# Kernel optimization log

Hardware: AMD Instinct MI355X
Metric: run time of the kernel (lower is better)

The kernel has to match this reference:

```python
import jax, jax.numpy as jnp
import numpy as np


def gcn_conv(x, W, b, src, dst, num_nodes):
    # PyG GCNConv: h = D^{-1/2} (A + I) D^{-1/2} (x W) + b
    h = x @ W  # [N, H]
    ones = jnp.ones(src.shape[0], dtype=h.dtype)
    deg = jax.ops.segment_sum(ones, dst, num_segments=num_nodes) + 1.0  # +1 for self-loop
    d_inv_sqrt = jax.lax.rsqrt(deg)
    norm = d_inv_sqrt[src] * d_inv_sqrt[dst]  # [E]
    msg = h[src] * norm[:, None]  # [E, H] gather
    agg = jax.ops.segment_sum(msg, dst, num_segments=num_nodes)  # scatter-add
    agg = agg + h * (1.0 / deg)[:, None]  # self-loop term: deg_i^{-1/2} * deg_i^{-1/2}
    return agg + b


def setup_inputs() -> dict:
    key = jax.random.key(0)
    ks = jax.random.split(key, 10)
    N, E, F, H, C, G = 100000, 1000000, 64, 128, 2, 512
    x = jax.random.normal(ks[0], (N, F), dtype=jnp.float32)
    edge_index = jax.random.randint(ks[1], (2, E), 0, N, dtype=jnp.int64)
    batch = jnp.sort(jax.random.randint(ks[2], (N,), 0, G, dtype=jnp.int64))
    s1 = 1.0 / np.sqrt(F)
    s2 = 1.0 / np.sqrt(H)
    W1 = jax.random.normal(ks[3], (F, H), dtype=jnp.float32) * s1
    b1 = jnp.zeros((H,), dtype=jnp.float32)
    W2 = jax.random.normal(ks[4], (H, H), dtype=jnp.float32) * s2
    b2 = jnp.zeros((H,), dtype=jnp.float32)
    Wfc = jax.random.normal(ks[5], (H, C), dtype=jnp.float32) * s2
    bfc = jnp.zeros((C,), dtype=jnp.float32)
    return {"x": x, "edge_index": edge_index, "batch": batch, "num_graphs": G,
            "W1": W1, "b1": b1, "W2": W2, "b2": b2, "Wfc": Wfc, "bfc": bfc}


def reference(x, edge_index, batch, num_graphs, W1, b1, W2, b2, Wfc, bfc):
    # Dropout is inference-mode (identity), matching model.eval().
    N = x.shape[0]
    src, dst = edge_index[0], edge_index[1]
    h = gcn_conv(x, W1, b1, src, dst, N)
    h = jax.nn.relu(h)
    h = gcn_conv(h, W2, b2, src, dst, N)
    h = jax.nn.relu(h)
    # global mean pool over graphs
    summed = jax.ops.segment_sum(h, batch, num_segments=num_graphs)  # [G, H]
    counts = jax.ops.segment_sum(jnp.ones((N,), h.dtype), batch, num_segments=num_graphs)
    pooled = summed / jnp.maximum(counts, 1.0)[:, None]
    logits = pooled @ Wfc + bfc  # [G, C]
    return jax.nn.softmax(logits, axis=1)
```

## Files before the change

### kernel.cpp

```cpp
#include <hip/hip_runtime.h>
#include <hip/hip_bf16.h>

typedef __hip_bfloat16 bf16;
typedef __attribute__((ext_vector_type(8))) short short8;
typedef __attribute__((ext_vector_type(4))) float f32x4;
typedef __attribute__((ext_vector_type(2))) float f32x2;

#define FDIM 64
#define HDIM 128
#define PROWS 256

#define ESTRIDE 4096
#define EC 8192
#define ECPT (EC / 256)

__device__ __forceinline__ float b2f(bf16 v) { return __bfloat162float(v); }
__device__ __forceinline__ float bits2f(unsigned int u) {
    return __uint_as_float(u << 16);
}
__device__ __forceinline__ unsigned short f2bits(float f) {
    bf16 b = __float2bfloat16(f);
    return *reinterpret_cast<unsigned short*>(&b);
}
__device__ __forceinline__ unsigned char f2fp8(float v) {
    int pk = __builtin_amdgcn_cvt_pk_fp8_f32(v, v, 0, false);
    return (unsigned char)(pk & 0xFF);
}

__global__ __launch_bounds__(256) void k_prep_flags(const unsigned short* __restrict__ w1u,
                                                    const int* __restrict__ edge,
                                                    const int* __restrict__ batch,
                                                    int* __restrict__ flags,
                                                    int* __restrict__ zbase, int zn4) {
    if (blockIdx.x == 0 && threadIdx.x < 192) {
        int wave = threadIdx.x >> 6, lane = threadIdx.x & 63;
        if (wave == 0) {
            int wild = 0;
#pragma unroll
            for (int r = 0; r < 2; r++) {
                int i = 2 * lane + 128 * r;
                int e = (w1u[i] >> 7) & 0xFF;
                wild += (e == 0 || e >= 137) ? 1 : 0;
            }
            for (int s = 32; s; s >>= 1) wild += __shfl_down(wild, s);
            if (lane == 0) flags[0] = (wild > 16) ? 1 : 0;
        } else if (wave == 1) {
            int z = 0;
#pragma unroll
            for (int r = 0; r < 2; r++) {
                int i = 2 * lane + 1 + 128 * r;
                z += (edge[i] == 0) ? 1 : 0;
            }
            for (int s = 32; s; s >>= 1) z += __shfl_down(z, s);
            if (lane == 0) flags[1] = (z > 64) ? 1 : 0;
        } else {
            int z = 0;
#pragma unroll
            for (int r = 0; r < 2; r++) {
                int i = 1025 + 2 * lane + 128 * r;
                z += (batch[i] == 0) ? 1 : 0;
            }
            for (int s = 32; s; s >>= 1) z += __shfl_down(z, s);
            if (lane == 0) flags[2] = (z > 64) ? 1 : 0;
        }
    }
    int4 zz = make_int4(0, 0, 0, 0);
    int stride = gridDim.x * 256;
    for (int t = blockIdx.x * 256 + threadIdx.x; t < zn4; t += stride)
        ((int4*)zbase)[t] = zz;
}

__device__ __forceinline__ int edge_word(const int* e, long long logical_idx, int is64) {
    return is64 ? e[2 * logical_idx] : e[logical_idx];
}

__global__ __launch_bounds__(256) void k_phase1(const int* __restrict__ edge,
                                                int* __restrict__ gcur,
                                                int* __restrict__ ebuf,
                                                int E,
                                                const void* __restrict__ W1, const void* __restrict__ b1,
                                                const void* __restrict__ W2, const void* __restrict__ b2,
                                                const void* __restrict__ Wfc, const void* __restrict__ bfc,
                                                bf16* __restrict__ W1t, bf16* __restrict__ W2t,
                                                bf16* __restrict__ b1c, bf16* __restrict__ b2c,
                                                bf16* __restrict__ Wfcc, bf16* __restrict__ bfcc,
                                                const void* __restrict__ x,
                                                unsigned char* __restrict__ X8,
                                                int totalX4, const int* __restrict__ flags,
                                                int NB1, int WB) {
    int blk = blockIdx.x;
    if (blk < NB1) {
        __shared__ int h[512];
        int tid = threadIdx.x;
        for (int b2 = tid; b2 < 512; b2 += 256) h[b2] = 0;
        __syncthreads();
        int is64 = flags[1];
        int e0 = blk * EC;
        int dcache[ECPT];
#pragma unroll
        for (int k = 0; k < ECPT; k++) {
            int i = e0 + (k << 8) + tid;
            int d = -1;
            if (i < E) d = edge_word(edge, (long long)E + i, is64);
            dcache[k] = d;
            if (d >= 0) atomicAdd(&h[(d >> 8) & 511], 1);
        }
        __syncthreads();
        for (int b2 = tid; b2 < 512; b2 += 256) {
            int c = h[b2];
            h[b2] = c ? atomicAdd(&gcur[b2], c) : 0;
        }
        __syncthreads();
#pragma unroll
        for (int k = 0; k < ECPT; k++) {
            int i = e0 + (k << 8) + tid;
            int d = dcache[k];
            if (d >= 0) {
                int s = edge_word(edge, i, is64);
                int bb = (d >> 8) & 511;
                int pos = atomicAdd(&h[bb], 1);
                if ((unsigned)pos < (unsigned)ESTRIDE)
                    ebuf[(bb << 12) + pos] = s | ((d & 255) << 24);
            }
        }
    } else if (blk < NB1 + WB) {
        int f0 = flags[0];
        int gid = (blk - NB1) * 256 + threadIdx.x;
        int stride = WB * 256;
#define CV(src, si) (f0 ? __float2bfloat16(((const float*)(src))[si]) : ((const bf16*)(src))[si])
        for (int i = gid; i < FDIM * HDIM; i += stride) {
            int n = i >> 6, k = i & 63;
            W1t[i] = CV(W1, k * HDIM + n);
        }
        for (int i = gid; i < HDIM * HDIM; i += stride) {
            int n = i >> 7, k = i & 127;
            W2t[i] = CV(W2, k * HDIM + n);
        }
        for (int i = gid; i < HDIM; i += stride) b1c[i] = CV(b1, i);
        for (int i = gid; i < HDIM; i += stride) b2c[i] = CV(b2, i);
        for (int i = gid; i < HDIM * 2; i += stride) Wfcc[i] = CV(Wfc, i);
        for (int i = gid; i < 2; i += stride) bfcc[i] = CV(bfc, i);
#undef CV
    } else {
        int t = (blk - NB1 - WB) * 256 + threadIdx.x;
        if (t >= totalX4) return;
        float4 v;
        if (flags[0]) {
            v = ((const float4*)x)[t];
        } else {
            uint2 p = ((const uint2*)x)[t];
            v.x = bits2f(p.x & 0xFFFFu); v.y = bits2f(p.x >> 16);
            v.z = bits2f(p.y & 0xFFFFu); v.w = bits2f(p.y >> 16);
        }
        unsigned int q0 = (unsigned int)__builtin_amdgcn_cvt_pk_fp8_f32(v.x, v.y, 0, false) & 0xFFFFu;
        unsigned int q1 = (unsigned int)__builtin_amdgcn_cvt_pk_fp8_f32(v.z, v.w, 0, false) & 0xFFFFu;
        ((unsigned int*)X8)[t] = (q1 << 16) | q0;
    }
}

__global__ __launch_bounds__(256) void k_csr(const int* __restrict__ ebuf,
                                             const int* __restrict__ gcur,
                                             int* __restrict__ rowptr,
                                             int* __restrict__ cnt,
                                             float* __restrict__ dinv,
                                             int* __restrict__ srclist,
                                             int N) {
    __shared__ int sred[256];
    __shared__ int sc[256];
    __shared__ int sa[256], sb[256];
    int b = blockIdx.x;
    int tid = threadIdx.x;
    int part = 0;
    for (int j = tid; j < b; j += 256) {
        int v = gcur[j];
        part += (v > ESTRIDE) ? ESTRIDE : v;
    }
    sred[tid] = part;
    __syncthreads();
    for (int s = 128; s > 0; s >>= 1) {
        if (tid < s) sred[tid] += sred[tid + s];
        __syncthreads();
    }
    int gbase = sred[0];
    int cnt_b = gcur[b];
    if (cnt_b > ESTRIDE) cnt_b = ESTRIDE;
    sc[tid] = 0;
    __syncthreads();
    const int* eb = ebuf + (b << 12);
    for (int j = tid; j < cnt_b; j += 256) {
        int p = eb[j];
        atomicAdd(&sc[(unsigned)p >> 24], 1);
    }
    __syncthreads();
    int cval = sc[tid];
    sa[tid] = cval;
    __syncthreads();
    int* cur = sa; int* nxt = sb;
    for (int off = 1; off < 256; off <<= 1) {
        int v = cur[tid];
        if (tid >= off) v += cur[tid - off];
        nxt[tid] = v;
        __syncthreads();
        int* t = cur; cur = nxt; nxt = t;
    }
    int excl = cur[tid] - cval;
    int node = (b << 8) + tid;
    if (node < N) {
        rowptr[node] = gbase + excl;
        cnt[node] = cval;
        dinv[node] = rsqrtf((float)cval + 1.0f);
    }
    __syncthreads();
    sc[tid] = excl;
    __syncthreads();
    for (int j = tid; j < cnt_b; j += 256) {
        int p = eb[j];
        int pos = atomicAdd(&sc[(unsigned)p >> 24], 1);
        srclist[gbase + pos] = p & 0xFFFFFF;
    }
}

#define ACCFP8(u2, e) do { \
    f32x2 f01 = __builtin_amdgcn_cvt_pk_f32_fp8((u2).x, false); \
    f32x2 f23 = __builtin_amdgcn_cvt_pk_f32_fp8((u2).x, true); \
    f32x2 f45 = __builtin_amdgcn_cvt_pk_f32_fp8((u2).y, false); \
    f32x2 f67 = __builtin_amdgcn_cvt_pk_f32_fp8((u2).y, true); \
    acc[0] += f01[0] * (e); acc[1] += f01[1] * (e); \
    acc[2] += f23[0] * (e); acc[3] += f23[1] * (e); \
    acc[4] += f45[0] * (e); acc[5] += f45[1] * (e); \
    acc[6] += f67[0] * (e); acc[7] += f67[1] * (e); } while (0)

__global__ __launch_bounds__(256) void k_agg64(const unsigned char* __restrict__ x8,
                                               const int* __restrict__ srclist,
                                               const int* __restrict__ rowptr,
                                               const int* __restrict__ count,
                                               const float* __restrict__ dinv,
                                               bf16* __restrict__ outb, int N) {
    int wave = threadIdx.x >> 6;
    int lane = threadIdx.x & 63;
    int group = lane >> 3;
    int sub = lane & 7;
    int i = blockIdx.x * 32 + wave * 8 + group;
    if (i >= N) return;
    int start = rowptr[i];
    int cnt = count[i];
    float di = dinv[i];
    const uint2* hrow = (const uint2*)x8;
    float acc[8] = {0.f, 0.f, 0.f, 0.f, 0.f, 0.f, 0.f, 0.f};
    int lb = group << 3;
    for (int jb = 0; jb < cnt; jb += 8) {
        int m = cnt - jb; if (m > 8) m = 8;
        int sv = srclist[start + jb + ((sub < m) ? sub : (m - 1))];
        float dvv = dinv[sv];
        int j = 0;
        for (; j + 4 <= m; j += 4) {
            int s0 = __shfl(sv, lb + j + 0); float e0 = __shfl(dvv, lb + j + 0);
            int s1 = __shfl(sv, lb + j + 1); float e1 = __shfl(dvv, lb + j + 1);
            int s2 = __shfl(sv, lb + j + 2); float e2 = __shfl(dvv, lb + j + 2);
            int s3 = __shfl(sv, lb + j + 3); float e3 = __shfl(dvv, lb + j + 3);
            uint2 v0 = hrow[(size_t)s0 * 8 + sub];
            uint2 v1 = hrow[(size_t)s1 * 8 + sub];
            uint2 v2 = hrow[(size_t)s2 * 8 + sub];
            uint2 v3 = hrow[(size_t)s3 * 8 + sub];
            ACCFP8(v0, e0); ACCFP8(v1, e1); ACCFP8(v2, e2); ACCFP8(v3, e3);
        }
        for (; j < m; j++) {
            int s0 = __shfl(sv, lb + j); float e0 = __shfl(dvv, lb + j);
            uint2 v0 = hrow[(size_t)s0 * 8 + sub];
            ACCFP8(v0, e0);
        }
    }
    {
        uint2 vs = hrow[(size_t)i * 8 + sub];
        float self = di * di;
        float sacc[8] = {0.f};
        {
            float* acc = sacc;
            ACCFP8(vs, self);
        }
#pragma unroll
        for (int k = 0; k < 8; k++) acc[k] = di * acc[k] + sacc[k];
    }
    uint4 pv;
    pv.x = ((unsigned int)f2bits(acc[1]) << 16) | f2bits(acc[0]);
    pv.y = ((unsigned int)f2bits(acc[3]) << 16) | f2bits(acc[2]);
    pv.z = ((unsigned int)f2bits(acc[5]) << 16) | f2bits(acc[4]);
    pv.w = ((unsigned int)f2bits(acc[7]) << 16) | f2bits(acc[6]);
    ((uint4*)outb)[(size_t)i * 8 + sub] = pv;
}

__global__ __launch_bounds__(256) void k_agg128(const unsigned char* __restrict__ h8,
                                                const int* __restrict__ srclist,
                                                const int* __restrict__ rowptr,
                                                const int* __restrict__ count,
                                                const float* __restrict__ dinv,
                                                bf16* __restrict__ outb, int N) {
    int wave = threadIdx.x >> 6;
    int lane = threadIdx.x & 63;
    int group = lane >> 4;
    int sub = lane & 15;
    int i = blockIdx.x * 16 + wave * 4 + group;
    if (i >= N) return;
    int start = rowptr[i];
    int cnt = count[i];
    float di = dinv[i];
    const uint2* hrow = (const uint2*)h8;
    float acc[8] = {0.f, 0.f, 0.f, 0.f, 0.f, 0.f, 0.f, 0.f};
    int lb = group << 4;
    for (int jb = 0; jb < cnt; jb += 16) {
        int m = cnt - jb; if (m > 16) m = 16;
        int sv = srclist[start + jb + ((sub < m) ? sub : (m - 1))];
        float dvv = dinv[sv];
        int j = 0;
        for (; j + 4 <= m; j += 4) {
            int s0 = __shfl(sv, lb + j + 0); float e0 = __shfl(dvv, lb + j + 0);
            int s1 = __shfl(sv, lb + j + 1); float e1 = __shfl(dvv, lb + j + 1);
            int s2 = __shfl(sv, lb + j + 2); float e2 = __shfl(dvv, lb + j + 2);
            int s3 = __shfl(sv, lb + j + 3); float e3 = __shfl(dvv, lb + j + 3);
            uint2 v0 = hrow[(size_t)s0 * 16 + sub];
            uint2 v1 = hrow[(size_t)s1 * 16 + sub];
            uint2 v2 = hrow[(size_t)s2 * 16 + sub];
            uint2 v3 = hrow[(size_t)s3 * 16 + sub];
            ACCFP8(v0, e0); ACCFP8(v1, e1); ACCFP8(v2, e2); ACCFP8(v3, e3);
        }
        for (; j < m; j++) {
            int s0 = __shfl(sv, lb + j); float e0 = __shfl(dvv, lb + j);
            uint2 v0 = hrow[(size_t)s0 * 16 + sub];
            ACCFP8(v0, e0);
        }
    }
    {
        uint2 vs = hrow[(size_t)i * 16 + sub];
        float self = di * di;
        float sacc[8] = {0.f};
        {
            float* acc = sacc;
            ACCFP8(vs, self);
        }
#pragma unroll
        for (int k = 0; k < 8; k++) acc[k] = di * acc[k] + sacc[k];
    }
    uint4 pv;
    pv.x = ((unsigned int)f2bits(acc[1]) << 16) | f2bits(acc[0]);
    pv.y = ((unsigned int)f2bits(acc[3]) << 16) | f2bits(acc[2]);
    pv.z = ((unsigned int)f2bits(acc[5]) << 16) | f2bits(acc[4]);
    pv.w = ((unsigned int)f2bits(acc[7]) << 16) | f2bits(acc[6]);
    ((uint4*)outb)[(size_t)i * 16 + sub] = pv;
}

#define K1PAD 72
__global__ __launch_bounds__(256) void k_gemmA(const bf16* __restrict__ Y,
                                               const bf16* __restrict__ W1t,
                                               const bf16* __restrict__ bias,
                                               unsigned char* __restrict__ h8, int N) {
    __shared__ bf16 As[64 * K1PAD];
    __shared__ bf16 Wt[HDIM * K1PAD];
    __shared__ float bsf[HDIM];
    int tid = threadIdx.x;
    int base = blockIdx.x * 64;
    {
        const uint4* wsrc = (const uint4*)W1t;
        for (int i = tid; i < HDIM * 8; i += 256) {
            int n = i >> 3, c = i & 7;
            *(uint4*)&Wt[n * K1PAD + c * 8] = wsrc[n * 8 + c];
        }
    }
    {
        const uint4* xb = (const uint4*)Y;
        for (int i = tid; i < 64 * 8; i += 256) {
            int r = i >> 3, c = i & 7;
            int gr = base + r; if (gr >= N) gr = N - 1;
            *(uint4*)&As[r * K1PAD + c * 8] = xb[(size_t)gr * 8 + c];
        }
    }
    if (tid < HDIM) bsf[tid] = b2f(bias[tid]);
    __syncthreads();
    int wid = tid >> 6, lane = tid & 63;
    int l15 = lane & 15, q = lane >> 4;
    int m0 = wid * 16;
    short8 af[2];
#pragma unroll
    for (int kc = 0; kc < 2; kc++)
        af[kc] = *(const short8*)&As[(m0 + l15) * K1PAD + kc * 32 + q * 8];
    f32x4 acc[8];
#pragma unroll
    for (int nt = 0; nt < 8; nt++) {
        acc[nt] = (f32x4){0.f, 0.f, 0.f, 0.f};
#pragma unroll
        for (int kc = 0; kc < 2; kc++) {
            short8 bf = *(const short8*)&Wt[(nt * 16 + l15) * K1PAD + kc * 32 + q * 8];
            acc[nt] = __builtin_amdgcn_mfma_f32_16x16x32_bf16(af[kc], bf, acc[nt], 0, 0, 0);
        }
    }
#pragma unroll
    for (int nt = 0; nt < 8; nt++) {
        int col = nt * 16 + l15;
        float bv = bsf[col];
#pragma unroll
        for (int r = 0; r < 4; r++) {
            int gr = base + m0 + q * 4 + r;
            if (gr < N) {
                float v = fmaxf(acc[nt][r] + bv, 0.f);
                h8[(size_t)gr * HDIM + col] = f2fp8(v);
            }
        }
    }
}

#define K2PAD 136
__global__ __launch_bounds__(256) void k_gemmB(const bf16* __restrict__ Z,
                                               const bf16* __restrict__ W2t,
                                               const bf16* __restrict__ bias,
                                               bf16* __restrict__ outp, int N) {
    __shared__ bf16 As[64 * K2PAD];
    __shared__ bf16 Wt[HDIM * K2PAD];
    __shared__ float bsf[HDIM];
    int tid = threadIdx.x;
    int base = blockIdx.x * 64;
    {
        const uint4* wsrc = (const uint4*)W2t;
        for (int i = tid; i < HDIM * 16; i += 256) {
            int n = i >> 4, c = i & 15;
            *(uint4*)&Wt[n * K2PAD + c * 8] = wsrc[n * 16 + c];
        }
    }
    const uint4* xb = (const uint4*)Z;
    for (int i = tid; i < 64 * 16; i += 256) {
        int r = i >> 4, c = i & 15;
        int gr = base + r; if (gr >= N) gr = N - 1;
        *(uint4*)&As[r * K2PAD + c * 8] = xb[(size_t)gr * 16 + c];
    }
    if (tid < HDIM) bsf[tid] = b2f(bias[tid]);
    __syncthreads();
    int wid = tid >> 6, lane = tid & 63;
    int l15 = lane & 15, q = lane >> 4;
    int m0 = wid * 16;
    short8 af[4];
#pragma unroll
    for (int kc = 0; kc < 4; kc++)
        af[kc] = *(const short8*)&As[(m0 + l15) * K2PAD + kc * 32 + q * 8];
    f32x4 acc[8];
#pragma unroll
    for (int nt = 0; nt < 8; nt++) {
        acc[nt] = (f32x4){0.f, 0.f, 0.f, 0.f};
#pragma unroll
        for (int kc = 0; kc < 4; kc++) {
            short8 bf = *(const short8*)&Wt[(nt * 16 + l15) * K2PAD + kc * 32 + q * 8];
            acc[nt] = __builtin_amdgcn_mfma_f32_16x16x32_bf16(af[kc], bf, acc[nt], 0, 0, 0);
        }
    }
#pragma unroll
    for (int nt = 0; nt < 8; nt++) {
        int col = nt * 16 + l15;
        float bv = bsf[col];
#pragma unroll
        for (int r = 0; r < 4; r++) {
            int gr = base + m0 + q * 4 + r;
            if (gr < N) outp[(size_t)gr * HDIM + col] = __float2bfloat16(fmaxf(acc[nt][r] + bv, 0.f));
        }
    }
}

__global__ __launch_bounds__(256) void k_pool_sum(const bf16* __restrict__ hact,
                                                  const int* __restrict__ batch,
                                                  float* __restrict__ Gsum,
                                                  float* __restrict__ Gcnt,
                                                  int N, const int* __restrict__ flags) {
    int wave = threadIdx.x >> 6, lane = threadIdx.x & 63;
    int base = blockIdx.x * PROWS;
    int is64 = flags[2];
    const unsigned int* hrow = (const unsigned int*)hact;
    float a0 = 0.f, a1 = 0.f;
    int c = 0, gcur = -1;
    for (int k = 0; k < PROWS / 4; k++) {
        int r = base + wave + 4 * k;
        if (r >= N) break;
        int g = is64 ? batch[2 * r] : batch[r];
        if (g != gcur) {
            if (gcur >= 0) {
                atomicAdd(&Gsum[gcur * HDIM + 2 * lane], a0);
                atomicAdd(&Gsum[gcur * HDIM + 2 * lane + 1], a1);
                if (lane == 0) atomicAdd(&Gcnt[gcur], (float)c);
            }
            a0 = a1 = 0.f; c = 0; gcur = g;
        }
        unsigned int v = hrow[(size_t)r * 64 + lane];
        a0 += bits2f(v & 0xFFFFu);
        a1 += bits2f(v >> 16);
        c++;
    }
    if (gcur >= 0) {
        atomicAdd(&Gsum[gcur * HDIM + 2 * lane], a0);
        atomicAdd(&Gsum[gcur * HDIM + 2 * lane + 1], a1);
        if (lane == 0) atomicAdd(&Gcnt[gcur], (float)c);
    }
}

__global__ __launch_bounds__(256) void k_pool_fc(const float* __restrict__ Gsum,
                                                 const float* __restrict__ Gcnt,
                                                 const bf16* __restrict__ Wfc,
                                                 const bf16* __restrict__ bfc,
                                                 void* __restrict__ out, int G,
                                                 const int* __restrict__ flags) {
    int wave = threadIdx.x >> 6, lane = threadIdx.x & 63;
    int g = blockIdx.x * 4 + wave;
    if (g >= G) return;
    float inv = 1.0f / fmaxf(Gcnt[g], 1.0f);
    float m0 = Gsum[g * HDIM + 2 * lane] * inv;
    float m1 = Gsum[g * HDIM + 2 * lane + 1] * inv;
    float l0 = m0 * b2f(Wfc[(2 * lane) * 2 + 0]) + m1 * b2f(Wfc[(2 * lane + 1) * 2 + 0]);
    float l1 = m0 * b2f(Wfc[(2 * lane) * 2 + 1]) + m1 * b2f(Wfc[(2 * lane + 1) * 2 + 1]);
    for (int s = 32; s; s >>= 1) { l0 += __shfl_down(l0, s); l1 += __shfl_down(l1, s); }
    if (lane == 0) {
        float z0 = l0 + b2f(bfc[0]);
        float z1 = l1 + b2f(bfc[1]);
        float mx = fmaxf(z0, z1);
        float e0 = expf(z0 - mx), e1 = expf(z1 - mx);
        float s = e0 + e1;
        float p0 = e0 / s, p1 = e1 / s;
        if (flags[0]) {
            ((float*)out)[2 * g + 0] = p0;
            ((float*)out)[2 * g + 1] = p1;
        } else {
            ((bf16*)out)[2 * g + 0] = __float2bfloat16(p0);
            ((bf16*)out)[2 * g + 1] = __float2bfloat16(p1);
        }
    }
}

extern "C" void kernel_launch(void* const* d_in, const int* in_sizes, int n_in,
                              void* d_out, int out_size, void* d_ws, size_t ws_size,
                              hipStream_t stream) {
    const void* x    = d_in[0];
    const int*  edge = (const int*)d_in[1];
    const int*  batch= (const int*)d_in[2];
    const void* W1  = d_in[4];
    const void* b1  = d_in[5];
    const void* W2  = d_in[6];
    const void* b2  = d_in[7];
    const void* Wfc = d_in[8];
    const void* bfc = d_in[9];

    int N = in_sizes[0] / FDIM;
    int E = in_sizes[1] / 2;
    int G = out_size / 2;

    int*   flags  = (int*)d_ws;
    float* dinv   = (float*)((char*)d_ws + 64);
    int*   gcur   = (int*)(dinv + N);
    float* Gsum   = (float*)(gcur + 512);
    float* Gcnt   = Gsum + (size_t)G * HDIM;
    int*   rowptr = (int*)(Gcnt + G);
    int*   count  = rowptr + N;
    int*   srclist= count + N;
    int*   ebuf   = srclist + E;
    bf16*  Abuf   = (bf16*)(ebuf + 512 * ESTRIDE);
    bf16*  Bbuf   = Abuf + (size_t)N * HDIM;
    bf16*  b1c    = Bbuf + (size_t)N * HDIM;
    bf16*  b2c    = b1c + HDIM;
    bf16*  Wfcc   = b2c + HDIM;
    bf16*  bfcc   = Wfcc + 256;
    bf16*  W1t    = bfcc + 64;
    bf16*  W2t    = W1t + FDIM * HDIM;
    unsigned char* H8 = (unsigned char*)(W2t + HDIM * HDIM);
    unsigned char* X8 = H8 + (size_t)N * HDIM;

    bf16* Y = Abuf;
    bf16* Z = Abuf;

    int NB  = (N + 255) >> 8;
    int NB1 = (E + EC - 1) / EC;
    int WB = 32;
    int XB = (N * 16 + 255) / 256;
    int totalX4 = N * 16;
    int zn4 = (512 + G * HDIM + G) / 4;

    k_prep_flags<<<64, 256, 0, stream>>>((const unsigned short*)W1, edge, batch, flags,
                                         gcur, zn4);
    k_phase1<<<NB1 + WB + XB, 256, 0, stream>>>(edge, gcur, ebuf, E,
                                                W1, b1, W2, b2, Wfc, bfc,
                                                W1t, W2t, b1c, b2c, Wfcc, bfcc,
                                                x, X8, totalX4, flags, NB1, WB);
    k_csr<<<NB, 256, 0, stream>>>(ebuf, gcur, rowptr, count, dinv, srclist, N);

    k_agg64<<<(N + 31) / 32, 256, 0, stream>>>(X8, srclist, rowptr, count, dinv, Y, N);
    k_gemmA<<<(N + 63) / 64, 256, 0, stream>>>(Y, W1t, b1c, H8, N);

    k_agg128<<<(N + 15) / 16, 256, 0, stream>>>(H8, srclist, rowptr, count, dinv, Z, N);
    k_gemmB<<<(N + 63) / 64, 256, 0, stream>>>(Z, W2t, b2c, Bbuf, N);

    k_pool_sum<<<(N + PROWS - 1) / PROWS, 256, 0, stream>>>(Bbuf, batch, Gsum, Gcnt, N, flags);
    k_pool_fc<<<(G + 3) / 4, 256, 0, stream>>>(Gsum, Gcnt, Wfcc, bfcc, d_out, G, flags);
}
```

Measured before the change: 250.5 us.

## Compute per-graph segment starts and pool one graph per block without atomics

Adds a stage to the phase-1 kernel that turns the sorted batch vector into per-graph start offsets. The pooling kernel then gives each graph its own block, which sums its rows with 16-byte loads and an LDS reduction and writes Gsum and Gcnt directly. This removes the float atomics and the zeroing of Gsum and Gcnt. It relies on batch being sorted, and block work becomes uneven if graph sizes differ.

```diff
diff --git a/kernel.cpp b/kernel.cpp
--- a/kernel.cpp
+++ b/kernel.cpp
@@ -8,7 +8,6 @@
 
 #define FDIM 64
 #define HDIM 128
-#define PROWS 256
 
 #define ESTRIDE 4096
 #define EC 8192
@@ -87,7 +86,10 @@
                                                 const void* __restrict__ x,
                                                 unsigned char* __restrict__ X8,
                                                 int totalX4, const int* __restrict__ flags,
-                                                int NB1, int WB) {
+                                                const int* __restrict__ batch,
+                                                int* __restrict__ gstart,
+                                                int N, int G,
+                                                int NB1, int WB, int XB) {
     int blk = blockIdx.x;
     if (blk < NB1) {
         __shared__ int h[512];
@@ -141,7 +143,7 @@
         for (int i = gid; i < HDIM * 2; i += stride) Wfcc[i] = CV(Wfc, i);
         for (int i = gid; i < 2; i += stride) bfcc[i] = CV(bfc, i);
 #undef CV
-    } else {
+    } else if (blk < NB1 + WB + XB) {
         int t = (blk - NB1 - WB) * 256 + threadIdx.x;
         if (t >= totalX4) return;
         float4 v;
@@ -155,6 +157,20 @@
         unsigned int q0 = (unsigned int)__builtin_amdgcn_cvt_pk_fp8_f32(v.x, v.y, 0, false) & 0xFFFFu;
         unsigned int q1 = (unsigned int)__builtin_amdgcn_cvt_pk_fp8_f32(v.z, v.w, 0, false) & 0xFFFFu;
         ((unsigned int*)X8)[t] = (q1 << 16) | q0;
+    } else {
+        int i = (blk - NB1 - WB - XB) * 256 + threadIdx.x;
+        if (i >= N) return;
+        int is64 = flags[2];
+        int bi = is64 ? batch[2 * i] : batch[i];
+        if (i == 0) {
+            for (int g = 0; g <= bi; g++) gstart[g] = 0;
+        } else {
+            int bp = is64 ? batch[2 * (i - 1)] : batch[i - 1];
+            for (int g = bp + 1; g <= bi; g++) gstart[g] = i;
+        }
+        if (i == N - 1) {
+            for (int g = bi + 1; g <= G; g++) gstart[g] = N;
+        }
     }
 }
 
@@ -462,37 +478,33 @@
 }
 
 __global__ __launch_bounds__(256) void k_pool_sum(const bf16* __restrict__ hact,
-                                                  const int* __restrict__ batch,
+                                                  const int* __restrict__ gstart,
                                                   float* __restrict__ Gsum,
-                                                  float* __restrict__ Gcnt,
-                                                  int N, const int* __restrict__ flags) {
-    int wave = threadIdx.x >> 6, lane = threadIdx.x & 63;
-    int base = blockIdx.x * PROWS;
-    int is64 = flags[2];
-    const unsigned int* hrow = (const unsigned int*)hact;
-    float a0 = 0.f, a1 = 0.f;
-    int c = 0, gcur = -1;
-    for (int k = 0; k < PROWS / 4; k++) {
-        int r = base + wave + 4 * k;
-        if (r >= N) break;
-        int g = is64 ? batch[2 * r] : batch[r];
-        if (g != gcur) {
-            if (gcur >= 0) {
-                atomicAdd(&Gsum[gcur * HDIM + 2 * lane], a0);
-                atomicAdd(&Gsum[gcur * HDIM + 2 * lane + 1], a1);
-                if (lane == 0) atomicAdd(&Gcnt[gcur], (float)c);
-            }
-            a0 = a1 = 0.f; c = 0; gcur = g;
-        }
-        unsigned int v = hrow[(size_t)r * 64 + lane];
-        a0 += bits2f(v & 0xFFFFu);
-        a1 += bits2f(v >> 16);
-        c++;
-    }
-    if (gcur >= 0) {
-        atomicAdd(&Gsum[gcur * HDIM + 2 * lane], a0);
-        atomicAdd(&Gsum[gcur * HDIM + 2 * lane + 1], a1);
-        if (lane == 0) atomicAdd(&Gcnt[gcur], (float)c);
+                                                  float* __restrict__ Gcnt) {
+    __shared__ float lds[16][HDIM + 1];
+    int g = blockIdx.x;
+    int s = gstart[g], e = gstart[g + 1];
+    int tid = threadIdx.x;
+    int cslot = tid & 15;
+    int rslot = tid >> 4;
+    const uint4* hp = (const uint4*)hact;
+    float a[8] = {0.f, 0.f, 0.f, 0.f, 0.f, 0.f, 0.f, 0.f};
+    for (int r = s + rslot; r < e; r += 16) {
+        uint4 v = hp[(size_t)r * 16 + cslot];
+        a[0] += bits2f(v.x & 0xFFFFu); a[1] += bits2f(v.x >> 16);
+        a[2] += bits2f(v.y & 0xFFFFu); a[3] += bits2f(v.y >> 16);
+        a[4] += bits2f(v.z & 0xFFFFu); a[5] += bits2f(v.z >> 16);
+        a[6] += bits2f(v.w & 0xFFFFu); a[7] += bits2f(v.w >> 16);
+    }
+#pragma unroll
+    for (int k = 0; k < 8; k++) lds[rslot][cslot * 8 + k] = a[k];
+    __syncthreads();
+    if (tid < HDIM) {
+        float sum = 0.f;
+#pragma unroll
+        for (int k = 0; k < 16; k++) sum += lds[k][tid];
+        Gsum[g * HDIM + tid] = sum;
+        if (tid == 0) Gcnt[g] = (float)(e - s);
     }
 }
 
@@ -548,7 +560,8 @@
     int*   flags  = (int*)d_ws;
     float* dinv   = (float*)((char*)d_ws + 64);
     int*   gcur   = (int*)(dinv + N);
-    float* Gsum   = (float*)(gcur + 512);
+    int*   gstart = gcur + 512;
+    float* Gsum   = (float*)(gstart + 516);
     float* Gcnt   = Gsum + (size_t)G * HDIM;
     int*   rowptr = (int*)(Gcnt + G);
     int*   count  = rowptr + N;
@@ -572,15 +585,18 @@
     int NB1 = (E + EC - 1) / EC;
     int WB = 32;
     int XB = (N * 16 + 255) / 256;
+    int BB = (N + 255) / 256;
     int totalX4 = N * 16;
-    int zn4 = (512 + G * HDIM + G) / 4;
+    int zn4 = 512 / 4;
 
     k_prep_flags<<<64, 256, 0, stream>>>((const unsigned short*)W1, edge, batch, flags,
                                          gcur, zn4);
-    k_phase1<<<NB1 + WB + XB, 256, 0, stream>>>(edge, gcur, ebuf, E,
-                                                W1, b1, W2, b2, Wfc, bfc,
-                                                W1t, W2t, b1c, b2c, Wfcc, bfcc,
-                                                x, X8, totalX4, flags, NB1, WB);
+    k_phase1<<<NB1 + WB + XB + BB, 256, 0, stream>>>(edge, gcur, ebuf, E,
+                                                     W1, b1, W2, b2, Wfc, bfc,
+                                                     W1t, W2t, b1c, b2c, Wfcc, bfcc,
+                                                     x, X8, totalX4, flags,
+                                                     batch, gstart, N, G,
+                                                     NB1, WB, XB);
     k_csr<<<NB, 256, 0, stream>>>(ebuf, gcur, rowptr, count, dinv, srclist, N);
 
     k_agg64<<<(N + 31) / 32, 256, 0, stream>>>(X8, srclist, rowptr, count, dinv, Y, N);
@@ -589,6 +605,6 @@
     k_agg128<<<(N + 15) / 16, 256, 0, stream>>>(H8, srclist, rowptr, count, dinv, Z, N);
     k_gemmB<<<(N + 63) / 64, 256, 0, stream>>>(Z, W2t, b2c, Bbuf, N);
 
-    k_pool_sum<<<(N + PROWS - 1) / PROWS, 256, 0, stream>>>(Bbuf, batch, Gsum, Gcnt, N, flags);
+    k_pool_sum<<<G, 256, 0, stream>>>(Bbuf, gstart, Gsum, Gcnt);
     k_pool_fc<<<(G + 3) / 4, 256, 0, stream>>>(Gsum, Gcnt, Wfcc, bfcc, d_out, G, flags);
 }
```

Result: faster. 223.6 us (-10.7%).
